# Performance work log

Hardware: AMD Instinct MI355X
Metric: run time of the kernel (lower is better)

Reference implementation:

```python
import jax, jax.numpy as jnp
import numpy as np
import math

B, NQ, NKV, D, H, KP = 4, 8192, 8192, 256, 8, 256
HD = D // H


def setup_inputs() -> dict:
    key = jax.random.key(0)
    ks = jax.random.split(key, 8)
    s = 1.0 / math.sqrt(D)
    return {
        "x1": jax.random.normal(ks[0], (B, NQ, D), dtype=jnp.float32),
        "x2": jax.random.normal(ks[1], (NKV, D), dtype=jnp.float32),
        "Wq": jax.random.normal(ks[2], (D, D), dtype=jnp.float32) * s,
        "Wk": jax.random.normal(ks[3], (D, D), dtype=jnp.float32) * s,
        "Wv": jax.random.normal(ks[4], (D, D), dtype=jnp.float32) * s,
        "Wo": jax.random.normal(ks[5], (D, D), dtype=jnp.float32) * s,
        "E": jax.random.normal(ks[6], (NKV, KP), dtype=jnp.float32) * (1.0 / math.sqrt(NKV)),
        "F": jax.random.normal(ks[7], (NKV, KP), dtype=jnp.float32) * (1.0 / math.sqrt(NKV)),
    }


def reference(x1, x2, Wq, Wk, Wv, Wo, E, F):
    # x1: [B, NQ, D] queries; x2: [NKV, D] shared cross-attention context
    q = x1 @ Wq                               # [B, NQ, D]
    k = x2 @ Wk                               # [NKV, D]
    v = x2 @ Wv                               # [NKV, D]
    # Linformer low-rank compression along the KV sequence axis
    k_low = jnp.einsum('nd,nk->kd', k, E)     # [KP, D]
    v_low = jnp.einsum('nd,nk->kd', v, F)     # [KP, D]
    qh = q.reshape(B, NQ, H, HD)
    kh = k_low.reshape(KP, H, HD)
    vh = v_low.reshape(KP, H, HD)
    scale = 1.0 / math.sqrt(HD)
    scores = jnp.einsum('bqhd,khd->bhqk', qh, kh) * scale  # [B, H, NQ, KP]
    attn = jax.nn.softmax(scores, axis=-1)
    out = jnp.einsum('bhqk,khd->bqhd', attn, vh)           # [B, NQ, H, HD]
    out = out.reshape(B, NQ, D)
    return out @ Wo
```

## Files before the change

### kernel.cpp

```cpp
#include <hip/hip_runtime.h>
#include <math.h>
#include <stdint.h>


typedef unsigned short ushort_t;
typedef __attribute__((ext_vector_type(8))) short bf16x8;
typedef __attribute__((ext_vector_type(8))) _Float16 f16x8;
typedef __attribute__((ext_vector_type(4))) float f32x4;

__device__ __forceinline__ f32x4 MFMA(bf16x8 a, bf16x8 b, f32x4 c) {
  return __builtin_amdgcn_mfma_f32_16x16x32_bf16(a, b, c, 0, 0, 0);
}
__device__ __forceinline__ f32x4 MFMA_H(f16x8 a, f16x8 b, f32x4 c) {
  return __builtin_amdgcn_mfma_f32_16x16x32_f16(a, b, c, 0, 0, 0);
}
__device__ __forceinline__ ushort_t f2bf(float x) {
  uint32_t u = __float_as_uint(x);
  u += 0x7fffu + ((u >> 16) & 1u);
  return (ushort_t)(u >> 16);
}
#define GLDS(gsrc, ldst)                                                    \
  __builtin_amdgcn_global_load_lds(                                         \
      (const __attribute__((address_space(1))) uint32_t*)(const void*)(gsrc), \
      (__attribute__((address_space(3))) uint32_t*)(void*)(ldst), 16, 0, 0)

#define STAGE_ROW(u) \
  (((((u) >> 2) ^ ((u) >> 4)) & 1) | (((u) >> 2) & 6) | (((u) >> 5) << 3))
#define STAGE_G(u) \
  ((((u) ^ ((u) >> 2) ^ ((u) >> 4)) & 1) | (((((u) >> 1) ^ ((u) >> 3)) & 1) << 1))

__global__ __launch_bounds__(256) void k_prep_all(
    const float* __restrict__ x2, const float* __restrict__ E,
    const float* __restrict__ F, const float* __restrict__ Wq,
    const float* __restrict__ Wk, const float* __restrict__ Wv,
    const float* __restrict__ Wo, _Float16* __restrict__ xt,
    ushort_t* __restrict__ wqt, ushort_t* __restrict__ wot,
    _Float16* __restrict__ wkt, _Float16* __restrict__ wvt) {
  __shared__ float tile[64][65];
  const int t = threadIdx.x;
  const int z = blockIdx.z;
  if (z < 3) {
    const int n0 = blockIdx.x * 64;
    const int c0 = blockIdx.y * 64;
    const float* __restrict__ src = (z == 0) ? x2 : (z == 1) ? E : F;
    _Float16* __restrict__ dst = xt + (size_t)z * 2097152;
    const int rr = t >> 4, cc = (t & 15) * 4;
#pragma unroll
    for (int i = 0; i < 4; ++i) {
      float4 v = *(const float4*)&src[(size_t)(n0 + rr + 16 * i) * 256 + c0 + cc];
      tile[cc + 0][rr + 16 * i] = v.x;
      tile[cc + 1][rr + 16 * i] = v.y;
      tile[cc + 2][rr + 16 * i] = v.z;
      tile[cc + 3][rr + 16 * i] = v.w;
    }
    __syncthreads();
#pragma unroll
    for (int rnd = 0; rnd < 2; ++rnd) {
      const int u = rnd * 256 + t;
      const int c = u >> 3, r0 = (u & 7) * 8;
      f16x8 h;
#pragma unroll
      for (int j = 0; j < 8; ++j) h[j] = (_Float16)tile[c][r0 + j];
      *(f16x8*)&dst[(size_t)(c0 + c) * 8192 + n0 + r0] = h;
    }
  } else {
    if (blockIdx.x >= 16) return;
    const int m = blockIdx.y;
    const float* __restrict__ src = (m == 0) ? Wq : (m == 1) ? Wo
                                  : (m == 2) ? Wk : Wv;
    const int tr = (blockIdx.x >> 2) * 64;
    const int tc = (blockIdx.x & 3) * 64;
    const int rr = t >> 4, cc = (t & 15) * 4;
#pragma unroll
    for (int i = 0; i < 4; ++i) {
      float4 v = *(const float4*)&src[(size_t)(tr + rr + 16 * i) * 256 + tc + cc];
      tile[cc + 0][rr + 16 * i] = v.x;
      tile[cc + 1][rr + 16 * i] = v.y;
      tile[cc + 2][rr + 16 * i] = v.z;
      tile[cc + 3][rr + 16 * i] = v.w;
    }
    __syncthreads();
#pragma unroll
    for (int rnd = 0; rnd < 2; ++rnd) {
      const int u = rnd * 256 + t;
      const int nl = u >> 3, kl = (u & 7) * 8;
      if (m < 2) {
        const float sc = (m == 0) ? 0.25503488f : 1.0f;
        bf16x8 hv;
#pragma unroll
        for (int j = 0; j < 8; ++j) hv[j] = (short)f2bf(tile[nl][kl + j] * sc);
        ushort_t* dst = (m == 0) ? wqt : wot;
        *(bf16x8*)&dst[(size_t)(tc + nl) * 256 + tr + kl] = hv;
      } else {
        f16x8 hv;
#pragma unroll
        for (int j = 0; j < 8; ++j) hv[j] = (_Float16)tile[nl][kl + j];
        _Float16* dst = (m == 2) ? wkt : wvt;
        *(f16x8*)&dst[(size_t)(tc + nl) * 256 + tr + kl] = hv;
      }
    }
  }
}

__global__ __launch_bounds__(256, 3) void k_mega1(
    const float* __restrict__ x1, const _Float16* __restrict__ xt,
    const ushort_t* __restrict__ wqt, ushort_t* __restrict__ Qf,
    float* __restrict__ part) {
  __shared__ __align__(16) char smem[32768];
  const int t = threadIdx.x;
  const int wv = t >> 6, ln = t & 63;
  const int l15 = ln & 15, g = ln >> 4;

  if (blockIdx.x < 512) {
    ushort_t* wstage = (ushort_t*)smem;
    const size_t r0 = (size_t)blockIdx.x * 64;
    auto stage = [&](int row0, int colu, int buf) {
#pragma unroll
      for (int rnd = 0; rnd < 2; ++rnd) {
        const int u = rnd * 256 + wv * 64 + ln;
        const int row = STAGE_ROW(u);
        const int gg = STAGE_G(u);
        GLDS(wqt + (size_t)(row0 + row) * 256 + colu + gg * 8,
             &wstage[(buf * 512 + rnd * 256 + wv * 64) * 8]);
      }
    };
    f32x4 qacc[16];
#pragma unroll
    for (int i = 0; i < 16; ++i) qacc[i] = {0.f, 0.f, 0.f, 0.f};
    stage(0, 0, 0);
    const float* xrow = x1 + (r0 + wv * 16 + l15) * 256;
    float4 xa = *(const float4*)(xrow + g * 8);
    float4 xb = *(const float4*)(xrow + g * 8 + 4);
    __syncthreads();
    for (int ci = 0; ci < 16; ++ci) {
      const int nh = ci & 1;
      if (ci < 15) stage(((ci + 1) & 1) * 128, ((ci + 1) >> 1) * 32, (ci + 1) & 1);
      bf16x8 afrag;
      afrag[0] = (short)f2bf(xa.x); afrag[1] = (short)f2bf(xa.y);
      afrag[2] = (short)f2bf(xa.z); afrag[3] = (short)f2bf(xa.w);
      afrag[4] = (short)f2bf(xb.x); afrag[5] = (short)f2bf(xb.y);
      afrag[6] = (short)f2bf(xb.z); afrag[7] = (short)f2bf(xb.w);
      const ushort_t* cw = &wstage[(ci & 1) * 4096];
#pragma unroll
      for (int tt = 0; tt < 8; ++tt) {
        bf16x8 bfr = *(const bf16x8*)&cw[((tt * 16 + l15) * 32 + g * 8) ^
                                         ((l15 & 7) << 3)];
        qacc[nh * 8 + tt] = MFMA(afrag, bfr, qacc[nh * 8 + tt]);
      }
      if (nh == 1 && ci < 15) {
        int ks = (ci >> 1) + 1;
        xa = *(const float4*)(xrow + ks * 32 + g * 8);
        xb = *(const float4*)(xrow + ks * 32 + g * 8 + 4);
      }
      __syncthreads();
    }
    char* myq = smem + wv * 8192;
#pragma unroll
    for (int tt = 0; tt < 16; ++tt)
#pragma unroll
      for (int r = 0; r < 4; ++r) {
        const int gr = g * 4 + r;
        *(ushort_t*)(myq + gr * 512 + (((tt * 16 + l15) * 2) ^ ((gr & 7) << 4))) =
            f2bf(qacc[tt][r]);
      }
    __builtin_amdgcn_sched_barrier(0);
    const int rt = blockIdx.x * 4 + wv;
#pragma unroll
    for (int hh = 0; hh < 8; ++hh) {
      bf16x8 qf = *(const bf16x8*)(myq + l15 * 512 +
                                   ((hh * 64 + g * 16) ^ ((l15 & 7) << 4)));
      *(bf16x8*)&Qf[((size_t)(rt * 8 + hh) * 64 + ln) * 8] = qf;
    }
  } else {
    const int bid = blockIdx.x - 512;
    const int which = bid & 1;
    const int chunk = (bid >> 1) & 15;
    const int quad = bid >> 5;
    const int kp0 = (quad >> 1) * 128;
    const int d0 = (quad & 1) * 128;
    const int n0 = chunk * 512;
    const _Float16* __restrict__ A = xt + (size_t)(1 + which) * 2097152;
    const _Float16* __restrict__ B = xt;
    const int wr = wv >> 1, wc = wv & 1;
    f32x4 acc[4][4];
#pragma unroll
    for (int i = 0; i < 4; ++i)
#pragma unroll
      for (int j = 0; j < 4; ++j) acc[i][j] = {0.f, 0.f, 0.f, 0.f};

    for (int ks = 0; ks < 8; ++ks) {
#pragma unroll
      for (int r8 = 0; r8 < 8; ++r8) {
        const int u = r8 * 256 + t;
        const int mm = u >> 10;
        const int uu = u & 1023;
        const int row = uu >> 3;
        const int nsw = ((uu ^ row) & 7) << 3;
        const _Float16* gs =
            (mm ? B + (size_t)(d0 + row) * 8192
                : A + (size_t)(kp0 + row) * 8192) +
            n0 + ks * 64 + nsw;
        GLDS(gs, smem + (u & ~63) * 16);
      }
      __syncthreads();
      const char* la = smem;
      const char* lb = smem + 16384;
#pragma unroll
      for (int kk = 0; kk < 2; ++kk) {
        f16x8 af[4], bf[4];
#pragma unroll
        for (int i = 0; i < 4; ++i) {
          const int ra = wr * 64 + i * 16 + l15;
          af[i] = *(const f16x8*)(la + ra * 128 +
                                  ((kk * 64 + g * 16) ^ ((ra & 7) << 4)));
        }
#pragma unroll
        for (int j = 0; j < 4; ++j) {
          const int rb = wc * 64 + j * 16 + l15;
          bf[j] = *(const f16x8*)(lb + rb * 128 +
                                  ((kk * 64 + g * 16) ^ ((rb & 7) << 4)));
        }
#pragma unroll
        for (int i = 0; i < 4; ++i)
#pragma unroll
          for (int j = 0; j < 4; ++j)
            acc[i][j] = MFMA_H(af[i], bf[j], acc[i][j]);
      }
      __syncthreads();
    }
    float* __restrict__ p = part + ((size_t)which * 16 + chunk) * 65536;
#pragma unroll
    for (int i = 0; i < 4; ++i)
#pragma unroll
      for (int j = 0; j < 4; ++j)
#pragma unroll
        for (int r = 0; r < 4; ++r)
          p[(size_t)(kp0 + wr * 64 + i * 16 + g * 4 + r) * 256 + d0 + wc * 64 +
            j * 16 + l15] = acc[i][j][r];
  }
}

__global__ __launch_bounds__(256) void k_reduce_part(
    const float* __restrict__ part, _Float16* __restrict__ ghh) {
  const int oid = blockIdx.x * 256 + threadIdx.x;
  const int which = oid >> 16;
  const int base = oid & 65535;
  const float* __restrict__ p = part + (size_t)which * 16 * 65536 + base;
  float s = 0.f;
#pragma unroll
  for (int c = 0; c < 16; ++c) s += p[c * 65536];
  ghh[oid] = (_Float16)s;
}

__global__ __launch_bounds__(256, 4) void k_lowproj2(
    const _Float16* __restrict__ ghh, const _Float16* __restrict__ wkt,
    const _Float16* __restrict__ wvt, ushort_t* __restrict__ klowA,
    ushort_t* __restrict__ vtb) {
  __shared__ __align__(16) _Float16 wstage[2][4096];
  const int t = threadIdx.x;
  const int wv = t >> 6, ln = t & 63;
  const int l15 = ln & 15, g = ln >> 4;
  const int which = blockIdx.y;
  const int r0 = blockIdx.x * 64;
  const _Float16* __restrict__ A = ghh + (size_t)which * 65536;
  const _Float16* __restrict__ W = which ? wvt : wkt;

  auto stage = [&](int row0, int colu, int buf) {
#pragma unroll
    for (int rnd = 0; rnd < 2; ++rnd) {
      const int u = rnd * 256 + wv * 64 + ln;
      const int row = STAGE_ROW(u);
      const int gg = STAGE_G(u);
      GLDS(W + (size_t)(row0 + row) * 256 + colu + gg * 8,
           &wstage[buf][(rnd * 256 + wv * 64) * 8]);
    }
  };

  f32x4 yacc[16];
#pragma unroll
  for (int i = 0; i < 16; ++i) yacc[i] = {0.f, 0.f, 0.f, 0.f};
  stage(0, 0, 0);
  const _Float16* arow = A + (size_t)(r0 + wv * 16 + l15) * 256;
  __syncthreads();
  for (int ci = 0; ci < 16; ++ci) {
    const int nh = ci & 1, ks = ci >> 1;
    if (ci < 15) stage(((ci + 1) & 1) * 128, ((ci + 1) >> 1) * 32, (ci + 1) & 1);
    f16x8 afrag = *(const f16x8*)(arow + ks * 32 + g * 8);
    const _Float16* cw = wstage[ci & 1];
#pragma unroll
    for (int tt = 0; tt < 8; ++tt) {
      f16x8 bfr = *(const f16x8*)&cw[((tt * 16 + l15) * 32 + g * 8) ^
                                     ((l15 & 7) << 3)];
      yacc[nh * 8 + tt] = MFMA_H(afrag, bfr, yacc[nh * 8 + tt]);
    }
    __syncthreads();
  }
#pragma unroll
  for (int tt = 0; tt < 16; ++tt)
#pragma unroll
    for (int r = 0; r < 4; ++r) {
      const int rowi = r0 + wv * 16 + g * 4 + r;
      const int c = tt * 16 + l15;
      const int hh = c >> 5, d = c & 31;
      const ushort_t val = f2bf(yacc[tt][r]);
      if (which == 0) {
        klowA[(hh << 13) + ((((rowi & 255) << 5) | d) ^ ((rowi & 7) << 3))] = val;
      } else {
        const int kh = (rowi >> 7) & 1, kl = rowi & 127;
        vtb[(((hh * 2 + kh) * 32 + d) << 7) + (kl ^ ((d & 7) << 3))] = val;
      }
    }
}

__global__ __launch_bounds__(512, 4) void k_attn(
    const ushort_t* __restrict__ Qf, const ushort_t* __restrict__ klowA,
    const ushort_t* __restrict__ vtb, ushort_t* __restrict__ O) {
  __shared__ __align__(16) ushort_t kv[16384];
  __shared__ __align__(16) uint32_t p_buf[8][320];
  __shared__ __align__(16) ushort_t o_sl[8][640];
  const int t = threadIdx.x;
  const int wv = t >> 6, ln = t & 63;
  const int l15 = ln & 15, g = ln >> 4;
  const int h = blockIdx.y;
  const size_t r0 = (size_t)blockIdx.x * 256;

  {
    const ushort_t* ksrc = klowA + h * 8192;
    const ushort_t* vsrc = vtb + h * 8192;
#pragma unroll
    for (int rnd = 0; rnd < 2; ++rnd) {
      const int ub = rnd * 512 + wv * 64;
      GLDS(ksrc + (ub + ln) * 8, &kv[ub * 8]);
    }
#pragma unroll
    for (int rnd = 0; rnd < 2; ++rnd) {
      const int ub = rnd * 512 + wv * 64;
      GLDS(vsrc + (ub + ln) * 8, &kv[8192 + ub * 8]);
    }
  }
  const int rtb = blockIdx.x * 16 + wv;
  bf16x8 qfA = *(const bf16x8*)&Qf[((size_t)(rtb * 8 + h) * 64 + ln) * 8];
  bf16x8 qfB = *(const bf16x8*)&Qf[((size_t)((rtb + 8) * 8 + h) * 64 + ln) * 8];
  __syncthreads();

#pragma unroll
  for (int st = 0; st < 2; ++st) {
    const bf16x8 qfrag = st ? qfB : qfA;
    f32x4 s[16];
#pragma unroll
    for (int tt = 0; tt < 16; ++tt) {
      bf16x8 kfr = *(const bf16x8*)&kv[((tt * 16 + l15) * 32 + g * 8) ^
                                       ((l15 & 7) << 3)];
      f32x4 z = {0.f, 0.f, 0.f, 0.f};
      s[tt] = MFMA(kfr, qfrag, z);
    }
    float sum = 0.f;
    uint32_t pw[16][2];
#pragma unroll
    for (int tt = 0; tt < 16; ++tt) {
      float e0 = exp2f(s[tt][0]), e1 = exp2f(s[tt][1]);
      float e2 = exp2f(s[tt][2]), e3 = exp2f(s[tt][3]);
      sum += (e0 + e1) + (e2 + e3);
      pw[tt][0] = (uint32_t)f2bf(e0) | ((uint32_t)f2bf(e1) << 16);
      pw[tt][1] = (uint32_t)f2bf(e2) | ((uint32_t)f2bf(e3) << 16);
    }
    sum += __shfl_xor(sum, 16);
    sum += __shfl_xor(sum, 32);
    const float rinv = 1.0f / sum;
    float rv[4];
#pragma unroll
    for (int r = 0; r < 4; ++r) rv[r] = __shfl(rinv, g * 4 + r);

    f32x4 oacc[2];
    oacc[0] = {0.f, 0.f, 0.f, 0.f};
    oacc[1] = {0.f, 0.f, 0.f, 0.f};
    uint32_t* pbw = &p_buf[wv][l15 * 20];
#pragma unroll
    for (int kh = 0; kh < 2; ++kh) {
      const char* cv = (const char*)&kv[8192 + kh * 4096];
#pragma unroll
      for (int ksl = 0; ksl < 4; ++ksl) {
        const int ks = kh * 4 + ksl;
        pbw[2 * g + 0] = pw[2 * ks][0];
        pbw[2 * g + 1] = pw[2 * ks][1];
        pbw[8 + 2 * g + 0] = pw[2 * ks + 1][0];
        pbw[8 + 2 * g + 1] = pw[2 * ks + 1][1];
        __builtin_amdgcn_sched_barrier(0);
        bf16x8 pfr = *(const bf16x8*)&p_buf[wv][l15 * 20 + 4 * g];
#pragma unroll
        for (int nt = 0; nt < 2; ++nt) {
          bf16x8 vfr = *(const bf16x8*)(cv + (nt * 16 + l15) * 256 +
                                        ((ksl * 64 + g * 16) ^ ((l15 & 7) << 4)));
          oacc[nt] = MFMA(pfr, vfr, oacc[nt]);
        }
        __builtin_amdgcn_sched_barrier(0);
      }
    }
#pragma unroll
    for (int nt = 0; nt < 2; ++nt)
#pragma unroll
      for (int r = 0; r < 4; ++r)
        o_sl[wv][(g * 4 + r) * 40 + nt * 16 + l15] = f2bf(oacc[nt][r] * rv[r]);
    __builtin_amdgcn_sched_barrier(0);
    {
      const int qr = ln >> 2, d0 = (ln & 3) * 8;
      bf16x8 ov = *(const bf16x8*)&o_sl[wv][qr * 40 + d0];
      *(bf16x8*)&O[(r0 + st * 128 + wv * 16 + qr) * 256 + h * 32 + d0] = ov;
    }
    __builtin_amdgcn_sched_barrier(0);
  }
}

__global__ __launch_bounds__(256, 4) void k_ogemm(
    const ushort_t* __restrict__ O, const ushort_t* __restrict__ wot,
    float* __restrict__ out) {
  __shared__ __align__(16) ushort_t wstage[2][4096];
  const int t = threadIdx.x;
  const int wv = t >> 6, ln = t & 63;
  const int l15 = ln & 15, g = ln >> 4;
  const size_t r0 = (size_t)blockIdx.x * 64;

  auto stage = [&](int row0, int colu, int buf) {
#pragma unroll
    for (int rnd = 0; rnd < 2; ++rnd) {
      const int u = rnd * 256 + wv * 64 + ln;
      const int row = STAGE_ROW(u);
      const int gg = STAGE_G(u);
      GLDS(wot + (size_t)(row0 + row) * 256 + colu + gg * 8,
           &wstage[buf][(rnd * 256 + wv * 64) * 8]);
    }
  };

  f32x4 yacc[16];
#pragma unroll
  for (int i = 0; i < 16; ++i) yacc[i] = {0.f, 0.f, 0.f, 0.f};
  stage(0, 0, 0);
  const ushort_t* arow = O + (r0 + wv * 16 + l15) * 256;
  __syncthreads();
  for (int ci = 0; ci < 16; ++ci) {
    const int nh = ci & 1, ks = ci >> 1;
    if (ci < 15) stage(((ci + 1) & 1) * 128, ((ci + 1) >> 1) * 32, (ci + 1) & 1);
    bf16x8 afrag = *(const bf16x8*)(arow + ks * 32 + g * 8);
    const ushort_t* cw = wstage[ci & 1];
#pragma unroll
    for (int tt = 0; tt < 8; ++tt) {
      bf16x8 bfr = *(const bf16x8*)&cw[((tt * 16 + l15) * 32 + g * 8) ^
                                       ((l15 & 7) << 3)];
      yacc[nh * 8 + tt] = MFMA(afrag, bfr, yacc[nh * 8 + tt]);
    }
    __syncthreads();
  }
#pragma unroll
  for (int tt = 0; tt < 16; ++tt)
#pragma unroll
    for (int r = 0; r < 4; ++r)
      out[(r0 + wv * 16 + g * 4 + r) * 256 + tt * 16 + l15] = yacc[tt][r];
}

extern "C" void kernel_launch(void* const* d_in, const int* in_sizes, int n_in,
                              void* d_out, int out_size, void* d_ws, size_t ws_size,
                              hipStream_t stream) {
  const float* x1 = (const float*)d_in[0];
  const float* x2 = (const float*)d_in[1];
  const float* Wq = (const float*)d_in[2];
  const float* Wk = (const float*)d_in[3];
  const float* Wv = (const float*)d_in[4];
  const float* Wo = (const float*)d_in[5];
  const float* E  = (const float*)d_in[6];
  const float* F  = (const float*)d_in[7];
  float* out = (float*)d_out;
  float* ws = (float*)d_ws;
  _Float16* ghh = (_Float16*)ws;
  ushort_t* wqt = (ushort_t*)(ws + 65536);
  ushort_t* wot = (ushort_t*)(ws + 98304);
  _Float16* wkt = (_Float16*)(ws + 131072);
  _Float16* wvt = (_Float16*)(ws + 163840);
  ushort_t* klowA = (ushort_t*)(ws + 196608);
  ushort_t* vtb = (ushort_t*)(ws + 229376);
  float* part = ws + 262144;
  ushort_t* Qf = (ushort_t*)(ws + 2359296);
  _Float16* xt = (_Float16*)(ws + 6553600);
  ushort_t* O = (ushort_t*)(ws + 6553600);

  k_prep_all<<<dim3(128, 4, 4), 256, 0, stream>>>(x2, E, F, Wq, Wk, Wv, Wo, xt,
                                                  wqt, wot, wkt, wvt);
  k_mega1<<<640, 256, 0, stream>>>(x1, xt, wqt, Qf, part);
  k_reduce_part<<<512, 256, 0, stream>>>(part, ghh);
  k_lowproj2<<<dim3(4, 2), 256, 0, stream>>>(ghh, wkt, wvt, klowA, vtb);
  k_attn<<<dim3(128, 8), 512, 0, stream>>>(Qf, klowA, vtb, O);
  k_ogemm<<<512, 256, 0, stream>>>(O, wot, out);
}
```

Baseline: 90.03 us.

## Use whole-weight LDS residency and larger tiles in Q, low-rank and output GEMMs

```diff
diff --git a/kernel.cpp b/kernel.cpp
--- a/kernel.cpp
+++ b/kernel.cpp
@@ -102,109 +102,55 @@
   }
 }
 
-__global__ __launch_bounds__(256, 3) void k_mega1(
+__global__ __launch_bounds__(512, 2) void k_mega1(
     const float* __restrict__ x1, const _Float16* __restrict__ xt,
     const ushort_t* __restrict__ wqt, ushort_t* __restrict__ Qf,
     float* __restrict__ part) {
-  __shared__ __align__(16) char smem[32768];
+  __shared__ __align__(16) char smem[131072];
   const int t = threadIdx.x;
   const int wv = t >> 6, ln = t & 63;
   const int l15 = ln & 15, g = ln >> 4;
 
-  if (blockIdx.x < 512) {
-    ushort_t* wstage = (ushort_t*)smem;
-    const size_t r0 = (size_t)blockIdx.x * 64;
-    auto stage = [&](int row0, int colu, int buf) {
-#pragma unroll
-      for (int rnd = 0; rnd < 2; ++rnd) {
-        const int u = rnd * 256 + wv * 64 + ln;
-        const int row = STAGE_ROW(u);
-        const int gg = STAGE_G(u);
-        GLDS(wqt + (size_t)(row0 + row) * 256 + colu + gg * 8,
-             &wstage[(buf * 512 + rnd * 256 + wv * 64) * 8]);
-      }
-    };
-    f32x4 qacc[16];
-#pragma unroll
-    for (int i = 0; i < 16; ++i) qacc[i] = {0.f, 0.f, 0.f, 0.f};
-    stage(0, 0, 0);
-    const float* xrow = x1 + (r0 + wv * 16 + l15) * 256;
-    float4 xa = *(const float4*)(xrow + g * 8);
-    float4 xb = *(const float4*)(xrow + g * 8 + 4);
-    __syncthreads();
-    for (int ci = 0; ci < 16; ++ci) {
-      const int nh = ci & 1;
-      if (ci < 15) stage(((ci + 1) & 1) * 128, ((ci + 1) >> 1) * 32, (ci + 1) & 1);
-      bf16x8 afrag;
-      afrag[0] = (short)f2bf(xa.x); afrag[1] = (short)f2bf(xa.y);
-      afrag[2] = (short)f2bf(xa.z); afrag[3] = (short)f2bf(xa.w);
-      afrag[4] = (short)f2bf(xb.x); afrag[5] = (short)f2bf(xb.y);
-      afrag[6] = (short)f2bf(xb.z); afrag[7] = (short)f2bf(xb.w);
-      const ushort_t* cw = &wstage[(ci & 1) * 4096];
-#pragma unroll
-      for (int tt = 0; tt < 8; ++tt) {
-        bf16x8 bfr = *(const bf16x8*)&cw[((tt * 16 + l15) * 32 + g * 8) ^
-                                         ((l15 & 7) << 3)];
-        qacc[nh * 8 + tt] = MFMA(afrag, bfr, qacc[nh * 8 + tt]);
-      }
-      if (nh == 1 && ci < 15) {
-        int ks = (ci >> 1) + 1;
-        xa = *(const float4*)(xrow + ks * 32 + g * 8);
-        xb = *(const float4*)(xrow + ks * 32 + g * 8 + 4);
-      }
-      __syncthreads();
-    }
-    char* myq = smem + wv * 8192;
-#pragma unroll
-    for (int tt = 0; tt < 16; ++tt)
-#pragma unroll
-      for (int r = 0; r < 4; ++r) {
-        const int gr = g * 4 + r;
-        *(ushort_t*)(myq + gr * 512 + (((tt * 16 + l15) * 2) ^ ((gr & 7) << 4))) =
-            f2bf(qacc[tt][r]);
-      }
-    __builtin_amdgcn_sched_barrier(0);
-    const int rt = blockIdx.x * 4 + wv;
-#pragma unroll
-    for (int hh = 0; hh < 8; ++hh) {
-      bf16x8 qf = *(const bf16x8*)(myq + l15 * 512 +
-                                   ((hh * 64 + g * 16) ^ ((l15 & 7) << 4)));
-      *(bf16x8*)&Qf[((size_t)(rt * 8 + hh) * 64 + ln) * 8] = qf;
-    }
-  } else {
-    const int bid = blockIdx.x - 512;
-    const int which = bid & 1;
-    const int chunk = (bid >> 1) & 15;
-    const int quad = bid >> 5;
-    const int kp0 = (quad >> 1) * 128;
-    const int d0 = (quad & 1) * 128;
+  if (blockIdx.x < 64) {
+    const int bid2 = blockIdx.x;
+    const int which = bid2 & 1;
+    const int chunk = (bid2 >> 1) & 15;
+    const int kp0 = (bid2 >> 5) * 128;
     const int n0 = chunk * 512;
     const _Float16* __restrict__ A = xt + (size_t)(1 + which) * 2097152;
     const _Float16* __restrict__ B = xt;
-    const int wr = wv >> 1, wc = wv & 1;
+    const int wr = wv >> 2, wc = wv & 3;
+
+    auto stage = [&](int buf, int ks) {
+#pragma unroll
+      for (int r6 = 0; r6 < 6; ++r6) {
+        const int u = r6 * 512 + t;
+        if (u < 1024) {
+          const int row = u >> 3, j = u & 7;
+          GLDS(A + (size_t)(kp0 + row) * 8192 + n0 + ks * 64 +
+                   ((j ^ (row & 7)) << 3),
+               smem + buf * 49152 + u * 16);
+        } else {
+          const int uu = u - 1024;
+          const int row = uu >> 3, j = uu & 7;
+          GLDS(B + (size_t)row * 8192 + n0 + ks * 64 + ((j ^ (row & 7)) << 3),
+               smem + buf * 49152 + 16384 + uu * 16);
+        }
+      }
+    };
+
     f32x4 acc[4][4];
 #pragma unroll
     for (int i = 0; i < 4; ++i)
 #pragma unroll
       for (int j = 0; j < 4; ++j) acc[i][j] = {0.f, 0.f, 0.f, 0.f};
 
+    stage(0, 0);
+    __syncthreads();
     for (int ks = 0; ks < 8; ++ks) {
-#pragma unroll
-      for (int r8 = 0; r8 < 8; ++r8) {
-        const int u = r8 * 256 + t;
-        const int mm = u >> 10;
-        const int uu = u & 1023;
-        const int row = uu >> 3;
-        const int nsw = ((uu ^ row) & 7) << 3;
-        const _Float16* gs =
-            (mm ? B + (size_t)(d0 + row) * 8192
-                : A + (size_t)(kp0 + row) * 8192) +
-            n0 + ks * 64 + nsw;
-        GLDS(gs, smem + (u & ~63) * 16);
-      }
-      __syncthreads();
-      const char* la = smem;
-      const char* lb = smem + 16384;
+      if (ks < 7) stage((ks + 1) & 1, ks + 1);
+      const char* la = smem + (ks & 1) * 49152;
+      const char* lb = la + 16384;
 #pragma unroll
       for (int kk = 0; kk < 2; ++kk) {
         f16x8 af[4], bf[4];
@@ -235,8 +181,81 @@
       for (int j = 0; j < 4; ++j)
 #pragma unroll
         for (int r = 0; r < 4; ++r)
-          p[(size_t)(kp0 + wr * 64 + i * 16 + g * 4 + r) * 256 + d0 + wc * 64 +
+          p[(size_t)(kp0 + wr * 64 + i * 16 + g * 4 + r) * 256 + wc * 64 +
             j * 16 + l15] = acc[i][j][r];
+  } else {
+    const int qb = blockIdx.x - 64;
+    const size_t r0 = (size_t)qb * 128;
+    ushort_t* wlds = (ushort_t*)smem;
+#pragma unroll
+    for (int rnd = 0; rnd < 16; ++rnd) {
+      const int u = rnd * 512 + t;
+      const int n = u >> 5, j = u & 31;
+      GLDS(wqt + ((size_t)n << 8) + ((j ^ (n & 7)) << 3), &wlds[u * 8]);
+    }
+    const int rg = wv >> 1, ch = wv & 1;
+    const float* xrowA = x1 + (r0 + rg * 32 + l15) * 256;
+    const float* xrowB = xrowA + 16 * 256;
+    f32x4 qacc[2][8];
+#pragma unroll
+    for (int s = 0; s < 2; ++s)
+#pragma unroll
+      for (int i = 0; i < 8; ++i) qacc[s][i] = {0.f, 0.f, 0.f, 0.f};
+    float4 a0 = *(const float4*)(xrowA + g * 8);
+    float4 a1 = *(const float4*)(xrowA + g * 8 + 4);
+    float4 b0 = *(const float4*)(xrowB + g * 8);
+    float4 b1 = *(const float4*)(xrowB + g * 8 + 4);
+    __syncthreads();
+
+    for (int ks = 0; ks < 8; ++ks) {
+      bf16x8 afA, afB;
+      afA[0] = (short)f2bf(a0.x); afA[1] = (short)f2bf(a0.y);
+      afA[2] = (short)f2bf(a0.z); afA[3] = (short)f2bf(a0.w);
+      afA[4] = (short)f2bf(a1.x); afA[5] = (short)f2bf(a1.y);
+      afA[6] = (short)f2bf(a1.z); afA[7] = (short)f2bf(a1.w);
+      afB[0] = (short)f2bf(b0.x); afB[1] = (short)f2bf(b0.y);
+      afB[2] = (short)f2bf(b0.z); afB[3] = (short)f2bf(b0.w);
+      afB[4] = (short)f2bf(b1.x); afB[5] = (short)f2bf(b1.y);
+      afB[6] = (short)f2bf(b1.z); afB[7] = (short)f2bf(b1.w);
+      if (ks < 7) {
+        a0 = *(const float4*)(xrowA + (ks + 1) * 32 + g * 8);
+        a1 = *(const float4*)(xrowA + (ks + 1) * 32 + g * 8 + 4);
+        b0 = *(const float4*)(xrowB + (ks + 1) * 32 + g * 8);
+        b1 = *(const float4*)(xrowB + (ks + 1) * 32 + g * 8 + 4);
+      }
+#pragma unroll
+      for (int tt = 0; tt < 8; ++tt) {
+        const int n = ch * 128 + tt * 16 + l15;
+        bf16x8 bfr = *(const bf16x8*)&wlds[(n << 8) +
+                                           ((((ks << 2) | g) ^ (n & 7)) << 3)];
+        qacc[0][tt] = MFMA(afA, bfr, qacc[0][tt]);
+        qacc[1][tt] = MFMA(afB, bfr, qacc[1][tt]);
+      }
+    }
+    __syncthreads();
+    char* myq = smem + wv * 8192;
+#pragma unroll
+    for (int s = 0; s < 2; ++s)
+#pragma unroll
+      for (int tt = 0; tt < 8; ++tt)
+#pragma unroll
+        for (int r = 0; r < 4; ++r) {
+          const int gr = g * 4 + r;
+          *(ushort_t*)(myq + s * 4096 + gr * 256 +
+                       (((tt * 16 + l15) * 2) ^ ((gr & 7) << 4))) =
+              f2bf(qacc[s][tt][r]);
+        }
+    __builtin_amdgcn_sched_barrier(0);
+#pragma unroll
+    for (int s = 0; s < 2; ++s) {
+      const int rt = qb * 8 + rg * 2 + s;
+#pragma unroll
+      for (int hl = 0; hl < 4; ++hl) {
+        bf16x8 qf = *(const bf16x8*)(myq + s * 4096 + l15 * 256 +
+                                     ((hl * 64 + g * 16) ^ ((l15 & 7) << 4)));
+        *(bf16x8*)&Qf[((size_t)(rt * 8 + ch * 4 + hl) * 64 + ln) * 8] = qf;
+      }
+    }
   }
 }
 
@@ -322,7 +341,7 @@
   const int wv = t >> 6, ln = t & 63;
   const int l15 = ln & 15, g = ln >> 4;
   const int h = blockIdx.y;
-  const size_t r0 = (size_t)blockIdx.x * 256;
+  const size_t r0 = (size_t)blockIdx.x * 512;
 
   {
     const ushort_t* ksrc = klowA + h * 8192;
@@ -338,14 +357,11 @@
       GLDS(vsrc + (ub + ln) * 8, &kv[8192 + ub * 8]);
     }
   }
-  const int rtb = blockIdx.x * 16 + wv;
-  bf16x8 qfA = *(const bf16x8*)&Qf[((size_t)(rtb * 8 + h) * 64 + ln) * 8];
-  bf16x8 qfB = *(const bf16x8*)&Qf[((size_t)((rtb + 8) * 8 + h) * 64 + ln) * 8];
   __syncthreads();
 
-#pragma unroll
-  for (int st = 0; st < 2; ++st) {
-    const bf16x8 qfrag = st ? qfB : qfA;
+  for (int st = 0; st < 4; ++st) {
+    const int rtb = blockIdx.x * 32 + st * 8 + wv;
+    const bf16x8 qfrag = *(const bf16x8*)&Qf[((size_t)(rtb * 8 + h) * 64 + ln) * 8];
     f32x4 s[16];
 #pragma unroll
     for (int tt = 0; tt < 16; ++tt) {
@@ -411,50 +427,55 @@
   }
 }
 
-__global__ __launch_bounds__(256, 4) void k_ogemm(
+__global__ __launch_bounds__(512, 2) void k_ogemm(
     const ushort_t* __restrict__ O, const ushort_t* __restrict__ wot,
     float* __restrict__ out) {
-  __shared__ __align__(16) ushort_t wstage[2][4096];
+  __shared__ __align__(16) ushort_t wlds[65536];
   const int t = threadIdx.x;
   const int wv = t >> 6, ln = t & 63;
   const int l15 = ln & 15, g = ln >> 4;
-  const size_t r0 = (size_t)blockIdx.x * 64;
-
-  auto stage = [&](int row0, int colu, int buf) {
-#pragma unroll
-    for (int rnd = 0; rnd < 2; ++rnd) {
-      const int u = rnd * 256 + wv * 64 + ln;
-      const int row = STAGE_ROW(u);
-      const int gg = STAGE_G(u);
-      GLDS(wot + (size_t)(row0 + row) * 256 + colu + gg * 8,
-           &wstage[buf][(rnd * 256 + wv * 64) * 8]);
-    }
-  };
-
-  f32x4 yacc[16];
-#pragma unroll
-  for (int i = 0; i < 16; ++i) yacc[i] = {0.f, 0.f, 0.f, 0.f};
-  stage(0, 0, 0);
-  const ushort_t* arow = O + (r0 + wv * 16 + l15) * 256;
+  const size_t r0 = (size_t)blockIdx.x * 128;
+#pragma unroll
+  for (int rnd = 0; rnd < 16; ++rnd) {
+    const int u = rnd * 512 + t;
+    const int n = u >> 5, j = u & 31;
+    GLDS(wot + ((size_t)n << 8) + ((j ^ (n & 7)) << 3), &wlds[u * 8]);
+  }
+  const int rg = wv >> 1, ch = wv & 1;
+  const ushort_t* arowA = O + (r0 + rg * 32 + l15) * 256;
+  const ushort_t* arowB = arowA + 16 * 256;
+  f32x4 yacc[2][8];
+#pragma unroll
+  for (int s = 0; s < 2; ++s)
+#pragma unroll
+    for (int i = 0; i < 8; ++i) yacc[s][i] = {0.f, 0.f, 0.f, 0.f};
+  bf16x8 afA = *(const bf16x8*)(arowA + g * 8);
+  bf16x8 afB = *(const bf16x8*)(arowB + g * 8);
   __syncthreads();
-  for (int ci = 0; ci < 16; ++ci) {
-    const int nh = ci & 1, ks = ci >> 1;
-    if (ci < 15) stage(((ci + 1) & 1) * 128, ((ci + 1) >> 1) * 32, (ci + 1) & 1);
-    bf16x8 afrag = *(const bf16x8*)(arow + ks * 32 + g * 8);
-    const ushort_t* cw = wstage[ci & 1];
+
+  for (int ks = 0; ks < 8; ++ks) {
+    bf16x8 cA = afA, cB = afB;
+    if (ks < 7) {
+      afA = *(const bf16x8*)(arowA + (ks + 1) * 32 + g * 8);
+      afB = *(const bf16x8*)(arowB + (ks + 1) * 32 + g * 8);
+    }
 #pragma unroll
     for (int tt = 0; tt < 8; ++tt) {
-      bf16x8 bfr = *(const bf16x8*)&cw[((tt * 16 + l15) * 32 + g * 8) ^
-                                       ((l15 & 7) << 3)];
-      yacc[nh * 8 + tt] = MFMA(afrag, bfr, yacc[nh * 8 + tt]);
-    }
-    __syncthreads();
-  }
-#pragma unroll
-  for (int tt = 0; tt < 16; ++tt)
-#pragma unroll
-    for (int r = 0; r < 4; ++r)
-      out[(r0 + wv * 16 + g * 4 + r) * 256 + tt * 16 + l15] = yacc[tt][r];
+      const int n = ch * 128 + tt * 16 + l15;
+      bf16x8 bfr = *(const bf16x8*)&wlds[(n << 8) +
+                                         ((((ks << 2) | g) ^ (n & 7)) << 3)];
+      yacc[0][tt] = MFMA(cA, bfr, yacc[0][tt]);
+      yacc[1][tt] = MFMA(cB, bfr, yacc[1][tt]);
+    }
+  }
+#pragma unroll
+  for (int s = 0; s < 2; ++s)
+#pragma unroll
+    for (int tt = 0; tt < 8; ++tt)
+#pragma unroll
+      for (int r = 0; r < 4; ++r)
+        out[(r0 + rg * 32 + s * 16 + g * 4 + r) * 256 + ch * 128 + tt * 16 +
+            l15] = yacc[s][tt][r];
 }
 
 extern "C" void kernel_launch(void* const* d_in, const int* in_sizes, int n_in,
@@ -484,9 +505,9 @@
 
   k_prep_all<<<dim3(128, 4, 4), 256, 0, stream>>>(x2, E, F, Wq, Wk, Wv, Wo, xt,
                                                   wqt, wot, wkt, wvt);
-  k_mega1<<<640, 256, 0, stream>>>(x1, xt, wqt, Qf, part);
+  k_mega1<<<320, 512, 0, stream>>>(x1, xt, wqt, Qf, part);
   k_reduce_part<<<512, 256, 0, stream>>>(part, ghh);
   k_lowproj2<<<dim3(4, 2), 256, 0, stream>>>(ghh, wkt, wvt, klowA, vtb);
-  k_attn<<<dim3(128, 8), 512, 0, stream>>>(Qf, klowA, vtb, O);
-  k_ogemm<<<512, 256, 0, stream>>>(O, wot, out);
-}
+  k_attn<<<dim3(64, 8), 512, 0, stream>>>(Qf, klowA, vtb, O);
+  k_ogemm<<<256, 512, 0, stream>>>(O, wot, out);
+}
```

Measured after the change: 94.66 us. 5.1% more time.

## Retile Q-projection, KV compression and output GEMM with 512-thread blocks and larger tiles

Applied to the files above, without the earlier changes.

```diff
diff --git a/kernel.cpp b/kernel.cpp
--- a/kernel.cpp
+++ b/kernel.cpp
@@ -102,55 +102,119 @@
   }
 }
 
-__global__ __launch_bounds__(256, 3) void k_mega1(
+__global__ __launch_bounds__(512, 2) void k_mega1(
     const float* __restrict__ x1, const _Float16* __restrict__ xt,
     const ushort_t* __restrict__ wqt, ushort_t* __restrict__ Qf,
     float* __restrict__ part) {
-  __shared__ __align__(16) char smem[32768];
+  __shared__ __align__(16) char smem[65536];
   const int t = threadIdx.x;
   const int wv = t >> 6, ln = t & 63;
   const int l15 = ln & 15, g = ln >> 4;
 
-  if (blockIdx.x < 512) {
-    ushort_t* wstage = (ushort_t*)smem;
-    const size_t r0 = (size_t)blockIdx.x * 64;
-    auto stage = [&](int row0, int colu, int buf) {
+  if (blockIdx.x < 64) {
+    const int bid2 = blockIdx.x;
+    const int which = bid2 & 1;
+    const int chunk = (bid2 >> 1) & 15;
+    const int kp0 = (bid2 >> 5) * 128;
+    const int n0 = chunk * 512;
+    const _Float16* __restrict__ A = xt + (size_t)(1 + which) * 2097152;
+    const _Float16* __restrict__ B = xt;
+    const int wr = wv >> 2, wc = wv & 3;
+
+    auto stage = [&](int buf, int st) {
+#pragma unroll
+      for (int r3 = 0; r3 < 3; ++r3) {
+        const int u = r3 * 512 + t;
+        if (u < 512) {
+          const int row = u >> 2, j = u & 3;
+          GLDS(A + (size_t)(kp0 + row) * 8192 + n0 + st * 32 +
+                   ((j ^ (row & 3)) << 3),
+               smem + buf * 24576 + u * 16);
+        } else {
+          const int uu = u - 512;
+          const int row = uu >> 2, j = uu & 3;
+          GLDS(B + (size_t)row * 8192 + n0 + st * 32 + ((j ^ (row & 3)) << 3),
+               smem + buf * 24576 + 8192 + uu * 16);
+        }
+      }
+    };
+
+    f32x4 acc[4][4];
+#pragma unroll
+    for (int i = 0; i < 4; ++i)
+#pragma unroll
+      for (int j = 0; j < 4; ++j) acc[i][j] = {0.f, 0.f, 0.f, 0.f};
+
+    stage(0, 0);
+    __syncthreads();
+    for (int st = 0; st < 16; ++st) {
+      if (st < 15) stage((st + 1) & 1, st + 1);
+      const char* la = smem + (st & 1) * 24576;
+      const char* lb = la + 8192;
+      f16x8 af[4], bf[4];
+#pragma unroll
+      for (int i = 0; i < 4; ++i) {
+        const int ra = wr * 64 + i * 16 + l15;
+        af[i] = *(const f16x8*)(la + ra * 64 + ((g ^ (ra & 3)) << 4));
+      }
+#pragma unroll
+      for (int j = 0; j < 4; ++j) {
+        const int rb = wc * 64 + j * 16 + l15;
+        bf[j] = *(const f16x8*)(lb + rb * 64 + ((g ^ (rb & 3)) << 4));
+      }
+#pragma unroll
+      for (int i = 0; i < 4; ++i)
+#pragma unroll
+        for (int j = 0; j < 4; ++j) acc[i][j] = MFMA_H(af[i], bf[j], acc[i][j]);
+      __syncthreads();
+    }
+    float* __restrict__ p = part + ((size_t)which * 16 + chunk) * 65536;
+#pragma unroll
+    for (int i = 0; i < 4; ++i)
+#pragma unroll
+      for (int j = 0; j < 4; ++j)
+#pragma unroll
+        for (int r = 0; r < 4; ++r)
+          p[(size_t)(kp0 + wr * 64 + i * 16 + g * 4 + r) * 256 + wc * 64 +
+            j * 16 + l15] = acc[i][j][r];
+  } else {
+    const int qb = blockIdx.x - 64;
+    const size_t r0 = (size_t)qb * 128;
+    auto stageq = [&](int buf, int ks) {
 #pragma unroll
       for (int rnd = 0; rnd < 2; ++rnd) {
-        const int u = rnd * 256 + wv * 64 + ln;
-        const int row = STAGE_ROW(u);
-        const int gg = STAGE_G(u);
-        GLDS(wqt + (size_t)(row0 + row) * 256 + colu + gg * 8,
-             &wstage[(buf * 512 + rnd * 256 + wv * 64) * 8]);
+        const int u = rnd * 512 + t;
+        const int n = u >> 2, j = u & 3;
+        GLDS(wqt + n * 256 + ks * 32 + ((j ^ (n & 3)) << 3),
+             smem + buf * 16384 + u * 16);
       }
     };
     f32x4 qacc[16];
 #pragma unroll
     for (int i = 0; i < 16; ++i) qacc[i] = {0.f, 0.f, 0.f, 0.f};
-    stage(0, 0, 0);
+    stageq(0, 0);
     const float* xrow = x1 + (r0 + wv * 16 + l15) * 256;
-    float4 xa = *(const float4*)(xrow + g * 8);
-    float4 xb = *(const float4*)(xrow + g * 8 + 4);
-    __syncthreads();
-    for (int ci = 0; ci < 16; ++ci) {
-      const int nh = ci & 1;
-      if (ci < 15) stage(((ci + 1) & 1) * 128, ((ci + 1) >> 1) * 32, (ci + 1) & 1);
+    float4 a0 = *(const float4*)(xrow + g * 8);
+    float4 a1 = *(const float4*)(xrow + g * 8 + 4);
+    __syncthreads();
+
+    for (int ks = 0; ks < 8; ++ks) {
+      if (ks < 7) stageq((ks + 1) & 1, ks + 1);
       bf16x8 afrag;
-      afrag[0] = (short)f2bf(xa.x); afrag[1] = (short)f2bf(xa.y);
-      afrag[2] = (short)f2bf(xa.z); afrag[3] = (short)f2bf(xa.w);
-      afrag[4] = (short)f2bf(xb.x); afrag[5] = (short)f2bf(xb.y);
-      afrag[6] = (short)f2bf(xb.z); afrag[7] = (short)f2bf(xb.w);
-      const ushort_t* cw = &wstage[(ci & 1) * 4096];
-#pragma unroll
-      for (int tt = 0; tt < 8; ++tt) {
-        bf16x8 bfr = *(const bf16x8*)&cw[((tt * 16 + l15) * 32 + g * 8) ^
-                                         ((l15 & 7) << 3)];
-        qacc[nh * 8 + tt] = MFMA(afrag, bfr, qacc[nh * 8 + tt]);
-      }
-      if (nh == 1 && ci < 15) {
-        int ks = (ci >> 1) + 1;
-        xa = *(const float4*)(xrow + ks * 32 + g * 8);
-        xb = *(const float4*)(xrow + ks * 32 + g * 8 + 4);
+      afrag[0] = (short)f2bf(a0.x); afrag[1] = (short)f2bf(a0.y);
+      afrag[2] = (short)f2bf(a0.z); afrag[3] = (short)f2bf(a0.w);
+      afrag[4] = (short)f2bf(a1.x); afrag[5] = (short)f2bf(a1.y);
+      afrag[6] = (short)f2bf(a1.z); afrag[7] = (short)f2bf(a1.w);
+      if (ks < 7) {
+        a0 = *(const float4*)(xrow + (ks + 1) * 32 + g * 8);
+        a1 = *(const float4*)(xrow + (ks + 1) * 32 + g * 8 + 4);
+      }
+      const char* cw = smem + (ks & 1) * 16384;
+#pragma unroll
+      for (int tt = 0; tt < 16; ++tt) {
+        bf16x8 bfr = *(const bf16x8*)(cw + (tt * 16 + l15) * 64 +
+                                      ((g ^ (l15 & 3)) << 4));
+        qacc[tt] = MFMA(afrag, bfr, qacc[tt]);
       }
       __syncthreads();
     }
@@ -160,83 +224,18 @@
 #pragma unroll
       for (int r = 0; r < 4; ++r) {
         const int gr = g * 4 + r;
-        *(ushort_t*)(myq + gr * 512 + (((tt * 16 + l15) * 2) ^ ((gr & 7) << 4))) =
+        *(ushort_t*)(myq + gr * 512 +
+                     (((tt * 16 + l15) * 2) ^ ((gr & 7) << 4))) =
             f2bf(qacc[tt][r]);
       }
     __builtin_amdgcn_sched_barrier(0);
-    const int rt = blockIdx.x * 4 + wv;
+    const int rt = qb * 8 + wv;
 #pragma unroll
     for (int hh = 0; hh < 8; ++hh) {
       bf16x8 qf = *(const bf16x8*)(myq + l15 * 512 +
                                    ((hh * 64 + g * 16) ^ ((l15 & 7) << 4)));
       *(bf16x8*)&Qf[((size_t)(rt * 8 + hh) * 64 + ln) * 8] = qf;
     }
-  } else {
-    const int bid = blockIdx.x - 512;
-    const int which = bid & 1;
-    const int chunk = (bid >> 1) & 15;
-    const int quad = bid >> 5;
-    const int kp0 = (quad >> 1) * 128;
-    const int d0 = (quad & 1) * 128;
-    const int n0 = chunk * 512;
-    const _Float16* __restrict__ A = xt + (size_t)(1 + which) * 2097152;
-    const _Float16* __restrict__ B = xt;
-    const int wr = wv >> 1, wc = wv & 1;
-    f32x4 acc[4][4];
-#pragma unroll
-    for (int i = 0; i < 4; ++i)
-#pragma unroll
-      for (int j = 0; j < 4; ++j) acc[i][j] = {0.f, 0.f, 0.f, 0.f};
-
-    for (int ks = 0; ks < 8; ++ks) {
-#pragma unroll
-      for (int r8 = 0; r8 < 8; ++r8) {
-        const int u = r8 * 256 + t;
-        const int mm = u >> 10;
-        const int uu = u & 1023;
-        const int row = uu >> 3;
-        const int nsw = ((uu ^ row) & 7) << 3;
-        const _Float16* gs =
-            (mm ? B + (size_t)(d0 + row) * 8192
-                : A + (size_t)(kp0 + row) * 8192) +
-            n0 + ks * 64 + nsw;
-        GLDS(gs, smem + (u & ~63) * 16);
-      }
-      __syncthreads();
-      const char* la = smem;
-      const char* lb = smem + 16384;
-#pragma unroll
-      for (int kk = 0; kk < 2; ++kk) {
-        f16x8 af[4], bf[4];
-#pragma unroll
-        for (int i = 0; i < 4; ++i) {
-          const int ra = wr * 64 + i * 16 + l15;
-          af[i] = *(const f16x8*)(la + ra * 128 +
-                                  ((kk * 64 + g * 16) ^ ((ra & 7) << 4)));
-        }
-#pragma unroll
-        for (int j = 0; j < 4; ++j) {
-          const int rb = wc * 64 + j * 16 + l15;
-          bf[j] = *(const f16x8*)(lb + rb * 128 +
-                                  ((kk * 64 + g * 16) ^ ((rb & 7) << 4)));
-        }
-#pragma unroll
-        for (int i = 0; i < 4; ++i)
-#pragma unroll
-          for (int j = 0; j < 4; ++j)
-            acc[i][j] = MFMA_H(af[i], bf[j], acc[i][j]);
-      }
-      __syncthreads();
-    }
-    float* __restrict__ p = part + ((size_t)which * 16 + chunk) * 65536;
-#pragma unroll
-    for (int i = 0; i < 4; ++i)
-#pragma unroll
-      for (int j = 0; j < 4; ++j)
-#pragma unroll
-        for (int r = 0; r < 4; ++r)
-          p[(size_t)(kp0 + wr * 64 + i * 16 + g * 4 + r) * 256 + d0 + wc * 64 +
-            j * 16 + l15] = acc[i][j][r];
   }
 }
 
@@ -322,7 +321,7 @@
   const int wv = t >> 6, ln = t & 63;
   const int l15 = ln & 15, g = ln >> 4;
   const int h = blockIdx.y;
-  const size_t r0 = (size_t)blockIdx.x * 256;
+  const size_t r0 = (size_t)blockIdx.x * 512;
 
   {
     const ushort_t* ksrc = klowA + h * 8192;
@@ -338,14 +337,11 @@
       GLDS(vsrc + (ub + ln) * 8, &kv[8192 + ub * 8]);
     }
   }
-  const int rtb = blockIdx.x * 16 + wv;
-  bf16x8 qfA = *(const bf16x8*)&Qf[((size_t)(rtb * 8 + h) * 64 + ln) * 8];
-  bf16x8 qfB = *(const bf16x8*)&Qf[((size_t)((rtb + 8) * 8 + h) * 64 + ln) * 8];
   __syncthreads();
 
-#pragma unroll
-  for (int st = 0; st < 2; ++st) {
-    const bf16x8 qfrag = st ? qfB : qfA;
+  for (int st = 0; st < 4; ++st) {
+    const int rtb = blockIdx.x * 32 + st * 8 + wv;
+    const bf16x8 qfrag = *(const bf16x8*)&Qf[((size_t)(rtb * 8 + h) * 64 + ln) * 8];
     f32x4 s[16];
 #pragma unroll
     for (int tt = 0; tt < 16; ++tt) {
@@ -411,42 +407,43 @@
   }
 }
 
-__global__ __launch_bounds__(256, 4) void k_ogemm(
+__global__ __launch_bounds__(512, 2) void k_ogemm(
     const ushort_t* __restrict__ O, const ushort_t* __restrict__ wot,
     float* __restrict__ out) {
-  __shared__ __align__(16) ushort_t wstage[2][4096];
+  __shared__ __align__(16) char smem[32768];
   const int t = threadIdx.x;
   const int wv = t >> 6, ln = t & 63;
   const int l15 = ln & 15, g = ln >> 4;
-  const size_t r0 = (size_t)blockIdx.x * 64;
-
-  auto stage = [&](int row0, int colu, int buf) {
-#pragma unroll
-    for (int rnd = 0; rnd < 2; ++rnd) {
-      const int u = rnd * 256 + wv * 64 + ln;
-      const int row = STAGE_ROW(u);
-      const int gg = STAGE_G(u);
-      GLDS(wot + (size_t)(row0 + row) * 256 + colu + gg * 8,
-           &wstage[buf][(rnd * 256 + wv * 64) * 8]);
+  const size_t r0 = (size_t)blockIdx.x * 128;
+
+  auto stageo = [&](int buf, int ks) {
+#pragma unroll
+    for (int rnd = 0; rnd < 2; ++rnd) {
+      const int u = rnd * 512 + t;
+      const int n = u >> 2, j = u & 3;
+      GLDS(wot + n * 256 + ks * 32 + ((j ^ (n & 3)) << 3),
+           smem + buf * 16384 + u * 16);
     }
   };
 
   f32x4 yacc[16];
 #pragma unroll
   for (int i = 0; i < 16; ++i) yacc[i] = {0.f, 0.f, 0.f, 0.f};
-  stage(0, 0, 0);
+  stageo(0, 0);
   const ushort_t* arow = O + (r0 + wv * 16 + l15) * 256;
+  bf16x8 afrag = *(const bf16x8*)(arow + g * 8);
   __syncthreads();
-  for (int ci = 0; ci < 16; ++ci) {
-    const int nh = ci & 1, ks = ci >> 1;
-    if (ci < 15) stage(((ci + 1) & 1) * 128, ((ci + 1) >> 1) * 32, (ci + 1) & 1);
-    bf16x8 afrag = *(const bf16x8*)(arow + ks * 32 + g * 8);
-    const ushort_t* cw = wstage[ci & 1];
-#pragma unroll
-    for (int tt = 0; tt < 8; ++tt) {
-      bf16x8 bfr = *(const bf16x8*)&cw[((tt * 16 + l15) * 32 + g * 8) ^
-                                       ((l15 & 7) << 3)];
-      yacc[nh * 8 + tt] = MFMA(afrag, bfr, yacc[nh * 8 + tt]);
+
+  for (int ks = 0; ks < 8; ++ks) {
+    if (ks < 7) stageo((ks + 1) & 1, ks + 1);
+    bf16x8 cA = afrag;
+    if (ks < 7) afrag = *(const bf16x8*)(arow + (ks + 1) * 32 + g * 8);
+    const char* cw = smem + (ks & 1) * 16384;
+#pragma unroll
+    for (int tt = 0; tt < 16; ++tt) {
+      bf16x8 bfr = *(const bf16x8*)(cw + (tt * 16 + l15) * 64 +
+                                    ((g ^ (l15 & 3)) << 4));
+      yacc[tt] = MFMA(cA, bfr, yacc[tt]);
     }
     __syncthreads();
   }
@@ -484,9 +481,9 @@
 
   k_prep_all<<<dim3(128, 4, 4), 256, 0, stream>>>(x2, E, F, Wq, Wk, Wv, Wo, xt,
                                                   wqt, wot, wkt, wvt);
-  k_mega1<<<640, 256, 0, stream>>>(x1, xt, wqt, Qf, part);
+  k_mega1<<<320, 512, 0, stream>>>(x1, xt, wqt, Qf, part);
   k_reduce_part<<<512, 256, 0, stream>>>(part, ghh);
   k_lowproj2<<<dim3(4, 2), 256, 0, stream>>>(ghh, wkt, wvt, klowA, vtb);
-  k_attn<<<dim3(128, 8), 512, 0, stream>>>(Qf, klowA, vtb, O);
-  k_ogemm<<<512, 256, 0, stream>>>(O, wot, out);
-}
+  k_attn<<<dim3(64, 8), 512, 0, stream>>>(Qf, klowA, vtb, O);
+  k_ogemm<<<256, 512, 0, stream>>>(O, wot, out);
+}
```

Result: slower. 94.43 us (+4.9%).
